# Kernel optimization log

Measured on AMD Instinct MI355X. Metric: run time of the kernel, lower is better.

## Reference

```python
import jax, jax.numpy as jnp
import numpy as np

B, S, D, H = 2, 2048, 1024, 16
DH = D // H

def setup_inputs() -> dict:
    key = jax.random.key(0)
    ks = jax.random.split(key, 12)
    inp = {
        'query': jax.random.normal(ks[0], (B, S, D), jnp.float32),
        'key':   jax.random.normal(ks[1], (B, S, D), jnp.float32),
        'value': jax.random.normal(ks[2], (B, S, D), jnp.float32),
        # causal mask: 1.0 where attention is DISALLOWED (added as mask * -1e9)
        'mask': jnp.triu(jnp.ones((S, S), jnp.float32), k=1)[None, None, :, :],
    }
    sc = 1.0 / np.sqrt(D)
    inp['Wq'] = jax.random.normal(ks[3], (D, D), jnp.float32) * sc
    inp['bq'] = jnp.zeros((D,), jnp.float32)
    inp['Wk'] = jax.random.normal(ks[4], (D, D), jnp.float32) * sc
    inp['bk'] = jnp.zeros((D,), jnp.float32)
    inp['Wv'] = jax.random.normal(ks[5], (D, D), jnp.float32) * sc
    inp['bv'] = jnp.zeros((D,), jnp.float32)
    inp['Wo'] = jax.random.normal(ks[6], (D, D), jnp.float32) * sc
    inp['bo'] = jnp.zeros((D,), jnp.float32)
    return inp

def _split_heads(x):
    # [B,S,D] -> [B,H,S,DH]
    b, s, _ = x.shape
    return x.reshape(b, s, H, DH).transpose(0, 2, 1, 3)

def reference(query, key, value, mask, Wq, bq, Wk, bk, Wv, bv, Wo, bo):
    q = _split_heads(query @ Wq + bq)
    k = _split_heads(key @ Wk + bk)
    v = _split_heads(value @ Wv + bv)
    scale = jnp.sqrt(jnp.asarray(DH, jnp.float32))
    # [B,H,S,S] score tensor (naive, unfused — matches original)
    score = jnp.einsum('bhqd,bhkd->bhqk', q, k) / scale
    score = score + mask * (-1e9)
    attn = jax.nn.softmax(score, axis=-1)
    ctx = jnp.einsum('bhqk,bhkd->bhqd', attn, v)
    ctx = ctx.transpose(0, 2, 1, 3).reshape(query.shape[0], -1, D)
    return ctx @ Wo + bo
```

## Files before the change

kernel.cpp:

```cpp
#include <hip/hip_runtime.h>
#include <hip/hip_bf16.h>
#include <stdint.h>


typedef __bf16 bf16;
typedef __bf16 bf16x2v __attribute__((ext_vector_type(2)));
typedef __bf16 bf16x4v __attribute__((ext_vector_type(4)));
typedef __bf16 bf16x8v __attribute__((ext_vector_type(8)));
typedef float  f32x4v  __attribute__((ext_vector_type(4)));
typedef float  f32x16v __attribute__((ext_vector_type(16)));
typedef unsigned int uint32x2v __attribute__((ext_vector_type(2)));

#define MFMA16(a, b, c) __builtin_amdgcn_mfma_f32_16x16x32_bf16((a), (b), (c), 0, 0, 0)
#define MFMA32(a, b, c) __builtin_amdgcn_mfma_f32_32x32x16_bf16((a), (b), (c), 0, 0, 0)

static constexpr int kS = 2048, kD = 1024, kH = 16, kDH = 64, kB = 2, kM = 4096;

__device__ __forceinline__ void gload16(const void* g, void* lds) {
  __builtin_amdgcn_global_load_lds((const __attribute__((address_space(1))) void*)g,
                                   (__attribute__((address_space(3))) void*)lds, 16, 0, 0);
}

__device__ __forceinline__ float fexp2(float x) {
#if __has_builtin(__builtin_amdgcn_exp2f)
  return __builtin_amdgcn_exp2f(x);
#else
  return exp2f(x);
#endif
}

__global__ void __launch_bounds__(256) cvt_x_kernel(
    const float* __restrict__ q, const float* __restrict__ k, const float* __restrict__ v,
    bf16* __restrict__ xq, bf16* __restrict__ xk, bf16* __restrict__ xv) {
  int i = (blockIdx.x * 256 + threadIdx.x) * 4;
  float4 a = *(const float4*)(q + i);
  float4 b = *(const float4*)(k + i);
  float4 c = *(const float4*)(v + i);
  bf16x4v oa = {(bf16)a.x, (bf16)a.y, (bf16)a.z, (bf16)a.w};
  bf16x4v ob = {(bf16)b.x, (bf16)b.y, (bf16)b.z, (bf16)b.w};
  bf16x4v oc = {(bf16)c.x, (bf16)c.y, (bf16)c.z, (bf16)c.w};
  *(bf16x4v*)(xq + i) = oa;
  *(bf16x4v*)(xk + i) = ob;
  *(bf16x4v*)(xv + i) = oc;
}

__global__ void __launch_bounds__(256) cvt_w_kernel(
    const float* __restrict__ w0, const float* __restrict__ w1,
    const float* __restrict__ w2, const float* __restrict__ w3,
    bf16* __restrict__ o0, bf16* __restrict__ o1, bf16* __restrict__ o2, bf16* __restrict__ o3) {
  const float* w = blockIdx.z == 0 ? w0 : blockIdx.z == 1 ? w1 : blockIdx.z == 2 ? w2 : w3;
  bf16* o       = blockIdx.z == 0 ? o0 : blockIdx.z == 1 ? o1 : blockIdx.z == 2 ? o2 : o3;
  __shared__ float t[32][33];
  int tx = threadIdx.x, ty = threadIdx.y;
  int k0 = blockIdx.x * 32, n0 = blockIdx.y * 32;
#pragma unroll
  for (int j = 0; j < 4; ++j)
    t[ty + j * 8][tx] = w[(size_t)(k0 + ty + j * 8) * kD + n0 + tx];
  __syncthreads();
#pragma unroll
  for (int j = 0; j < 4; ++j)
    o[(size_t)(n0 + ty + j * 8) * kD + k0 + tx] = (bf16)t[tx][ty + j * 8];
}

struct GemmArgs {
  const bf16* A;
  const bf16* Wt;
  const float* bias;
  void* out;
  float scale;
  int omode;
};

__global__ void __launch_bounds__(256) gemm_kernel(GemmArgs ga, GemmArgs gb, GemmArgs gc) {
  GemmArgs g = blockIdx.z == 0 ? ga : blockIdx.z == 1 ? gb : gc;
  __shared__ bf16 smem[8192];
  const int tid = threadIdx.x;
  const int wid = tid >> 6, lane = tid & 63;
  const int g4 = lane >> 4, l16 = lane & 15;
  const int m0 = blockIdx.x * 128, n0 = blockIdx.y * 128;
  const int wr = wid >> 1, wc = wid & 1;

  const int row0 = wid * 16 + (lane >> 2);
  const int row1 = 64 + row0;
  const int sw0 = (lane & 3) ^ ((row0 >> 1) & 3);
  const int sw1 = (lane & 3) ^ ((row1 >> 1) & 3);
  const bf16* gA0 = g.A + (size_t)(m0 + row0) * kD + sw0 * 8;
  const bf16* gA1 = g.A + (size_t)(m0 + row1) * kD + sw1 * 8;
  const bf16* gB0 = g.Wt + (size_t)(n0 + row0) * kD + sw0 * 8;
  const bf16* gB1 = g.Wt + (size_t)(n0 + row1) * kD + sw1 * 8;
  bf16* ldsA0 = &smem[wid * 512];
  bf16* ldsA1 = &smem[(4 + wid) * 512];
  bf16* ldsB0 = &smem[4096 + wid * 512];
  bf16* ldsB1 = &smem[4096 + (4 + wid) * 512];

  const int xorv = (l16 >> 1) & 3;
  f32x4v acc[4][4] = {};

  for (int k0 = 0; k0 < kD; k0 += 32) {
    __syncthreads();
    gload16(gA0 + k0, ldsA0);
    gload16(gA1 + k0, ldsA1);
    gload16(gB0 + k0, ldsB0);
    gload16(gB1 + k0, ldsB1);
    __syncthreads();
    bf16x8v af[4], bfr[4];
#pragma unroll
    for (int i = 0; i < 4; ++i) {
      int rowA = wr * 64 + i * 16 + l16;
      af[i] = *(const bf16x8v*)&smem[rowA * 32 + ((g4 ^ xorv) * 8)];
      int rowB = wc * 64 + i * 16 + l16;
      bfr[i] = *(const bf16x8v*)&smem[4096 + rowB * 32 + ((g4 ^ xorv) * 8)];
    }
#pragma unroll
    for (int i = 0; i < 4; ++i)
#pragma unroll
      for (int j = 0; j < 4; ++j)
        acc[i][j] = MFMA16(af[i], bfr[j], acc[i][j]);
  }

#pragma unroll
  for (int j = 0; j < 4; ++j) {
    int col = n0 + wc * 64 + j * 16 + l16;
    float bj = g.bias[col];
#pragma unroll
    for (int i = 0; i < 4; ++i) {
#pragma unroll
      for (int r = 0; r < 4; ++r) {
        int m = m0 + wr * 64 + i * 16 + g4 * 4 + r;
        float val = (acc[i][j][r] + bj) * g.scale;
        if (g.omode == 0) {
          ((float*)g.out)[(size_t)m * kD + col] = val;
        } else {
          int b = m >> 11, s = m & (kS - 1);
          int h = col >> 6, dh = col & 63;
          size_t addr = (g.omode == 1)
                            ? (((size_t)(b * kH + h) * kS + s) * kDH + dh)
                            : (((size_t)(b * kH + h) * kDH + dh) * kS + s);
          ((bf16*)g.out)[addr] = (bf16)val;
        }
      }
    }
  }
}

__global__ void __launch_bounds__(256) attn_kernel(
    const bf16* __restrict__ Qp, const bf16* __restrict__ Kp,
    const bf16* __restrict__ Vt, bf16* __restrict__ ctx) {
  __shared__ bf16 lds[16384];
  const int tid = threadIdx.x;
  const int wid = tid >> 6, lane = tid & 63;
  const int l32 = lane & 31, hi = lane >> 5;
  const int bh = blockIdx.x;
  const int qt = blockIdx.y;
  const int q0 = qt * 128;
  const int qw = q0 + wid * 32;
  const bf16* Qh = Qp + (size_t)bh * kS * kDH;
  const bf16* Kh = Kp + (size_t)bh * kS * kDH;
  const bf16* Vh = Vt + (size_t)bh * kDH * kS;

  bf16x8v qf[4];
#pragma unroll
  for (int kw = 0; kw < 4; ++kw)
    qf[kw] = *(const bf16x8v*)(Qh + (size_t)(qw + l32) * kDH + kw * 16 + hi * 8);

  f32x16v oacc[2] = {};
  float mreg = -1e30f, lsum = 0.f;
  const int q_lane = qw + l32;

  const int nt = (q0 >> 6) + 2;
  const int ntw = (qw >> 6) + 1;

  const int srow = lane >> 3, schk = lane & 7;
  auto stage = [&](int buf, int k0) {
    bf16* kd = &lds[buf * 8192];
    bf16* vd = kd + 4096;
#pragma unroll
    for (int i = 0; i < 2; ++i) {
      int r = wid * 16 + i * 8 + srow;
      int c = schk ^ (r & 7);
      gload16(Kh + (size_t)(k0 + r) * kDH + c * 8, kd + (wid * 2 + i) * 512);
      gload16(Vh + (size_t)r * kS + k0 + c * 8, vd + (wid * 2 + i) * 512);
    }
  };

  stage(0, 0);
  __syncthreads();
  int cur = 0;
  for (int t = 0; t < nt; ++t) {
    const int k0 = t * 64;
    if (t + 1 < nt) stage(cur ^ 1, k0 + 64);
    if (t < ntw) {
      const bf16* kb = &lds[cur * 8192];
      const bf16* vb = kb + 4096;
      f32x16v st[2] = {};
#pragma unroll
      for (int sub = 0; sub < 2; ++sub) {
        int row = sub * 32 + l32;
        const bf16* krow = kb + row * 64;
        int rx = row & 7;
#pragma unroll
        for (int kw = 0; kw < 4; ++kw) {
          int cw = kw * 2 + hi;
          bf16x8v af = *(const bf16x8v*)(krow + ((cw ^ rx) * 8));
          st[sub] = MFMA32(af, qf[kw], st[sub]);
        }
      }
      if (k0 + 63 > qw) {
#pragma unroll
        for (int sub = 0; sub < 2; ++sub)
#pragma unroll
          for (int r = 0; r < 16; ++r) {
            int kv = k0 + sub * 32 + (r & 3) + 8 * (r >> 2) + 4 * hi;
            if (kv > q_lane) st[sub][r] = -1e30f;
          }
      }
      float rm = st[0][0];
#pragma unroll
      for (int sub = 0; sub < 2; ++sub)
#pragma unroll
        for (int r = 0; r < 16; ++r) rm = fmaxf(rm, st[sub][r]);
      {
        uint32x2v sw = __builtin_amdgcn_permlane32_swap(
            __float_as_uint(rm), __float_as_uint(rm), false, false);
        float partner = __uint_as_float(hi ? sw.x : sw.y);
        rm = fmaxf(rm, partner);
      }
      float mn = fmaxf(mreg, rm);
      float al = fexp2(mreg - mn);
      mreg = mn;
      float rs = 0.f;
#pragma unroll
      for (int sub = 0; sub < 2; ++sub)
#pragma unroll
        for (int r = 0; r < 16; ++r) {
          st[sub][r] = fexp2(st[sub][r] - mn);
          rs += st[sub][r];
        }
      {
        uint32x2v sw = __builtin_amdgcn_permlane32_swap(
            __float_as_uint(rs), __float_as_uint(rs), false, false);
        rs += __uint_as_float(hi ? sw.x : sw.y);
      }
      lsum = lsum * al + rs;
#pragma unroll
      for (int s = 0; s < 2; ++s)
#pragma unroll
        for (int r = 0; r < 16; ++r) oacc[s][r] *= al;

      unsigned int w[16];
#pragma unroll
      for (int sub = 0; sub < 2; ++sub)
#pragma unroll
        for (int i = 0; i < 8; ++i) {
          union { bf16x2v h; unsigned int u; } cv;
          cv.h = bf16x2v{(bf16)st[sub][2 * i], (bf16)st[sub][2 * i + 1]};
          w[sub * 8 + i] = cv.u;
        }
      bf16x8v pb[4];
#pragma unroll
      for (int f = 0; f < 4; ++f) {
        uint32x2v r0 = __builtin_amdgcn_permlane32_swap(w[4 * f], w[4 * f + 2], false, false);
        uint32x2v r1 = __builtin_amdgcn_permlane32_swap(w[4 * f + 1], w[4 * f + 3], false, false);
        union { unsigned int u[4]; bf16x8v h; } fu;
        fu.u[0] = r0.x; fu.u[1] = r1.x; fu.u[2] = r0.y; fu.u[3] = r1.y;
        pb[f] = fu.h;
      }
#pragma unroll
      for (int f = 0; f < 4; ++f) {
        int cw = f * 2 + hi;
#pragma unroll
        for (int s = 0; s < 2; ++s) {
          int row = s * 32 + l32;
          bf16x8v vf = *(const bf16x8v*)(vb + row * 64 + ((cw ^ (row & 7)) * 8));
          oacc[s] = MFMA32(vf, pb[f], oacc[s]);
        }
      }
    }
    __syncthreads();
    cur ^= 1;
  }
  float inv = 1.0f / lsum;
  const int b = bh >> 4, h = bh & 15;
  bf16* crow = ctx + (size_t)(b * kS + qw + l32) * kD + h * 64;
#pragma unroll
  for (int s = 0; s < 2; ++s)
#pragma unroll
    for (int rq = 0; rq < 4; ++rq) {
      union { bf16x4v h; uint32x2v u; } pk;
      pk.h = bf16x4v{(bf16)(oacc[s][rq * 4 + 0] * inv), (bf16)(oacc[s][rq * 4 + 1] * inv),
                     (bf16)(oacc[s][rq * 4 + 2] * inv), (bf16)(oacc[s][rq * 4 + 3] * inv)};
      *(uint32x2v*)(crow + 8 * rq + 4 * hi + 32 * s) = pk.u;
    }
}

extern "C" void kernel_launch(void* const* d_in, const int* in_sizes, int n_in,
                              void* d_out, int out_size, void* d_ws, size_t ws_size,
                              hipStream_t stream) {
  (void)in_sizes; (void)n_in; (void)out_size; (void)ws_size;
  const float* q  = (const float*)d_in[0];
  const float* k  = (const float*)d_in[1];
  const float* v  = (const float*)d_in[2];
  const float* Wq = (const float*)d_in[4];
  const float* bq = (const float*)d_in[5];
  const float* Wk = (const float*)d_in[6];
  const float* bk = (const float*)d_in[7];
  const float* Wv = (const float*)d_in[8];
  const float* bv = (const float*)d_in[9];
  const float* Wo = (const float*)d_in[10];
  const float* bo = (const float*)d_in[11];

  char* p = (char*)d_ws;
  auto carve = [&](size_t bytes) {
    char* r = p;
    p += (bytes + 255) & ~(size_t)255;
    return r;
  };
  const size_t XB = (size_t)kM * kD * sizeof(bf16);
  const size_t WB = (size_t)kD * kD * sizeof(bf16);
  bf16* Xq  = (bf16*)carve(XB);
  bf16* Xk  = (bf16*)carve(XB);
  bf16* Xv  = (bf16*)carve(XB);
  bf16* Wtq = (bf16*)carve(WB);
  bf16* Wtk = (bf16*)carve(WB);
  bf16* Wtv = (bf16*)carve(WB);
  bf16* Wto = (bf16*)carve(WB);
  bf16* Qp  = (bf16*)carve(XB);
  bf16* Kp  = (bf16*)carve(XB);
  bf16* Vt  = (bf16*)carve(XB);
  bf16* Ctx = (bf16*)carve(XB);

  cvt_x_kernel<<<dim3(kM * kD / 1024), 256, 0, stream>>>(q, k, v, Xq, Xk, Xv);
  cvt_w_kernel<<<dim3(32, 32, 4), dim3(32, 8, 1), 0, stream>>>(Wq, Wk, Wv, Wo,
                                                               Wtq, Wtk, Wtv, Wto);
  GemmArgs aq{Xq, Wtq, bq, Qp, 0.125f * 1.44269504f, 1};
  GemmArgs ak{Xk, Wtk, bk, Kp, 1.0f, 1};
  GemmArgs av{Xv, Wtv, bv, Vt, 1.0f, 2};
  gemm_kernel<<<dim3(32, 8, 3), 256, 0, stream>>>(aq, ak, av);
  attn_kernel<<<dim3(32, 16), 256, 0, stream>>>(Qp, Kp, Vt, Ctx);
  GemmArgs ao{Ctx, Wto, bo, d_out, 1.0f, 0};
  gemm_kernel<<<dim3(32, 8, 1), 256, 0, stream>>>(ao, ao, ao);
}
```

Baseline: 243.2 us.

## Fuse fp32 activation cast into projection GEMM, stage epilogues, widen attention KV tiles

```diff
diff --git a/kernel.cpp b/kernel.cpp
--- a/kernel.cpp
+++ b/kernel.cpp
@@ -11,10 +11,11 @@
 typedef float  f32x16v __attribute__((ext_vector_type(16)));
 typedef unsigned int uint32x2v __attribute__((ext_vector_type(2)));
 
+#define MFMA32(a, b, c) __builtin_amdgcn_mfma_f32_32x32x16_bf16((a), (b), (c), 0, 0, 0)
 #define MFMA16(a, b, c) __builtin_amdgcn_mfma_f32_16x16x32_bf16((a), (b), (c), 0, 0, 0)
-#define MFMA32(a, b, c) __builtin_amdgcn_mfma_f32_32x32x16_bf16((a), (b), (c), 0, 0, 0)
-
-static constexpr int kS = 2048, kD = 1024, kH = 16, kDH = 64, kB = 2, kM = 4096;
+#define LGKM0() asm volatile("s_waitcnt lgkmcnt(0)" ::: "memory")
+
+static constexpr int kS = 2048, kD = 1024, kH = 16, kDH = 64, kM = 4096;
 
 __device__ __forceinline__ void gload16(const void* g, void* lds) {
   __builtin_amdgcn_global_load_lds((const __attribute__((address_space(1))) void*)g,
@@ -27,21 +28,6 @@
 #else
   return exp2f(x);
 #endif
-}
-
-__global__ void __launch_bounds__(256) cvt_x_kernel(
-    const float* __restrict__ q, const float* __restrict__ k, const float* __restrict__ v,
-    bf16* __restrict__ xq, bf16* __restrict__ xk, bf16* __restrict__ xv) {
-  int i = (blockIdx.x * 256 + threadIdx.x) * 4;
-  float4 a = *(const float4*)(q + i);
-  float4 b = *(const float4*)(k + i);
-  float4 c = *(const float4*)(v + i);
-  bf16x4v oa = {(bf16)a.x, (bf16)a.y, (bf16)a.z, (bf16)a.w};
-  bf16x4v ob = {(bf16)b.x, (bf16)b.y, (bf16)b.z, (bf16)b.w};
-  bf16x4v oc = {(bf16)c.x, (bf16)c.y, (bf16)c.z, (bf16)c.w};
-  *(bf16x4v*)(xq + i) = oa;
-  *(bf16x4v*)(xk + i) = ob;
-  *(bf16x4v*)(xv + i) = oc;
 }
 
 __global__ void __launch_bounds__(256) cvt_w_kernel(
@@ -63,7 +49,7 @@
 }
 
 struct GemmArgs {
-  const bf16* A;
+  const void* A;
   const bf16* Wt;
   const float* bias;
   void* out;
@@ -71,74 +57,160 @@
   int omode;
 };
 
+template <int BN, bool AFP32>
 __global__ void __launch_bounds__(256) gemm_kernel(GemmArgs ga, GemmArgs gb, GemmArgs gc) {
   GemmArgs g = blockIdx.z == 0 ? ga : blockIdx.z == 1 ? gb : gc;
-  __shared__ bf16 smem[8192];
-  const int tid = threadIdx.x;
-  const int wid = tid >> 6, lane = tid & 63;
+  constexpr int WN = BN / 2, NJ = WN / 16;
+  __shared__ __align__(16) char smem_raw[18432];
+  bf16* As = (bf16*)smem_raw;
+  bf16* Bs = (bf16*)(smem_raw + 8192);
+  const int tid = threadIdx.x, wid = tid >> 6, lane = tid & 63;
   const int g4 = lane >> 4, l16 = lane & 15;
-  const int m0 = blockIdx.x * 128, n0 = blockIdx.y * 128;
+  const int m0 = blockIdx.x * 128, n0 = blockIdx.y * BN;
   const int wr = wid >> 1, wc = wid & 1;
-
-  const int row0 = wid * 16 + (lane >> 2);
-  const int row1 = 64 + row0;
-  const int sw0 = (lane & 3) ^ ((row0 >> 1) & 3);
-  const int sw1 = (lane & 3) ^ ((row1 >> 1) & 3);
-  const bf16* gA0 = g.A + (size_t)(m0 + row0) * kD + sw0 * 8;
-  const bf16* gA1 = g.A + (size_t)(m0 + row1) * kD + sw1 * 8;
-  const bf16* gB0 = g.Wt + (size_t)(n0 + row0) * kD + sw0 * 8;
-  const bf16* gB1 = g.Wt + (size_t)(n0 + row1) * kD + sw1 * 8;
-  bf16* ldsA0 = &smem[wid * 512];
-  bf16* ldsA1 = &smem[(4 + wid) * 512];
-  bf16* ldsB0 = &smem[4096 + wid * 512];
-  bf16* ldsB1 = &smem[4096 + (4 + wid) * 512];
+  const bf16* Wt = g.Wt;
+
+  const int ar = tid >> 1, ah = tid & 1;
+  const float* gAf = (const float*)g.A + (size_t)(m0 + ar) * kD + ah * 16;
+  bf16* adst0 = As + ar * 32 + ((2 * ah) ^ ((ar >> 1) & 3)) * 8;
+  bf16* adst1 = As + ar * 32 + ((2 * ah + 1) ^ ((ar >> 1) & 3)) * 8;
 
   const int xorv = (l16 >> 1) & 3;
-  f32x4v acc[4][4] = {};
+  f32x4v acc[4][NJ] = {};
 
   for (int k0 = 0; k0 < kD; k0 += 32) {
     __syncthreads();
-    gload16(gA0 + k0, ldsA0);
-    gload16(gA1 + k0, ldsA1);
-    gload16(gB0 + k0, ldsB0);
-    gload16(gB1 + k0, ldsB1);
+    if constexpr (AFP32) {
+      float4 f0 = *(const float4*)(gAf + k0);
+      float4 f1 = *(const float4*)(gAf + k0 + 4);
+      float4 f2 = *(const float4*)(gAf + k0 + 8);
+      float4 f3 = *(const float4*)(gAf + k0 + 12);
+#pragma unroll
+      for (int i = 0; i < BN / 64; ++i) {
+        int id = i * 256 + tid;
+        int row = id >> 2, c = id & 3;
+        gload16(Wt + (size_t)(n0 + row) * kD + k0 + ((c ^ ((row >> 1) & 3)) * 8),
+                Bs + (i * 256 + wid * 64) * 8);
+      }
+      bf16x8v c0 = {(bf16)f0.x, (bf16)f0.y, (bf16)f0.z, (bf16)f0.w,
+                    (bf16)f1.x, (bf16)f1.y, (bf16)f1.z, (bf16)f1.w};
+      bf16x8v c1 = {(bf16)f2.x, (bf16)f2.y, (bf16)f2.z, (bf16)f2.w,
+                    (bf16)f3.x, (bf16)f3.y, (bf16)f3.z, (bf16)f3.w};
+      *(bf16x8v*)adst0 = c0;
+      *(bf16x8v*)adst1 = c1;
+    } else {
+      const bf16* Ab = (const bf16*)g.A;
+#pragma unroll
+      for (int i = 0; i < 2; ++i) {
+        int id = i * 256 + tid;
+        int row = id >> 2, c = id & 3;
+        gload16(Ab + (size_t)(m0 + row) * kD + k0 + ((c ^ ((row >> 1) & 3)) * 8),
+                As + (i * 256 + wid * 64) * 8);
+      }
+#pragma unroll
+      for (int i = 0; i < BN / 64; ++i) {
+        int id = i * 256 + tid;
+        int row = id >> 2, c = id & 3;
+        gload16(Wt + (size_t)(n0 + row) * kD + k0 + ((c ^ ((row >> 1) & 3)) * 8),
+                Bs + (i * 256 + wid * 64) * 8);
+      }
+    }
     __syncthreads();
-    bf16x8v af[4], bfr[4];
+    bf16x8v af[4], bfr[NJ];
 #pragma unroll
     for (int i = 0; i < 4; ++i) {
       int rowA = wr * 64 + i * 16 + l16;
-      af[i] = *(const bf16x8v*)&smem[rowA * 32 + ((g4 ^ xorv) * 8)];
-      int rowB = wc * 64 + i * 16 + l16;
-      bfr[i] = *(const bf16x8v*)&smem[4096 + rowB * 32 + ((g4 ^ xorv) * 8)];
+      af[i] = *(const bf16x8v*)(As + rowA * 32 + ((g4 ^ xorv) * 8));
+    }
+#pragma unroll
+    for (int j = 0; j < NJ; ++j) {
+      int rowB = wc * WN + j * 16 + l16;
+      bfr[j] = *(const bf16x8v*)(Bs + rowB * 32 + ((g4 ^ xorv) * 8));
     }
 #pragma unroll
     for (int i = 0; i < 4; ++i)
 #pragma unroll
-      for (int j = 0; j < 4; ++j)
+      for (int j = 0; j < NJ; ++j)
         acc[i][j] = MFMA16(af[i], bfr[j], acc[i][j]);
   }
 
-#pragma unroll
-  for (int j = 0; j < 4; ++j) {
-    int col = n0 + wc * 64 + j * 16 + l16;
-    float bj = g.bias[col];
+  __syncthreads();
+  float* bws = (float*)smem_raw + wid * 1152;
+  const int bb = m0 >> 11;
+
+  if (g.omode == 1) {
+    const int h = (n0 >> 6) + wc;
+    float bj[NJ];
+#pragma unroll
+    for (int j = 0; j < NJ; ++j) bj[j] = g.bias[n0 + wc * WN + j * 16 + l16];
 #pragma unroll
     for (int i = 0; i < 4; ++i) {
 #pragma unroll
-      for (int r = 0; r < 4; ++r) {
-        int m = m0 + wr * 64 + i * 16 + g4 * 4 + r;
-        float val = (acc[i][j][r] + bj) * g.scale;
-        if (g.omode == 0) {
-          ((float*)g.out)[(size_t)m * kD + col] = val;
-        } else {
-          int b = m >> 11, s = m & (kS - 1);
-          int h = col >> 6, dh = col & 63;
-          size_t addr = (g.omode == 1)
-                            ? (((size_t)(b * kH + h) * kS + s) * kDH + dh)
-                            : (((size_t)(b * kH + h) * kDH + dh) * kS + s);
-          ((bf16*)g.out)[addr] = (bf16)val;
-        }
-      }
+      for (int j = 0; j < NJ; ++j)
+#pragma unroll
+        for (int r = 0; r < 4; ++r)
+          bws[(g4 * 4 + r) * 68 + j * 16 + l16] = (acc[i][j][r] + bj[j]) * g.scale;
+      LGKM0();
+      int rr = lane & 15, q = lane >> 4;
+      const float* src = bws + rr * 68 + q * 16;
+      f32x4v v0 = *(const f32x4v*)(src);
+      f32x4v v1 = *(const f32x4v*)(src + 4);
+      f32x4v v2 = *(const f32x4v*)(src + 8);
+      f32x4v v3 = *(const f32x4v*)(src + 12);
+      bf16x8v o0 = {(bf16)v0.x, (bf16)v0.y, (bf16)v0.z, (bf16)v0.w,
+                    (bf16)v1.x, (bf16)v1.y, (bf16)v1.z, (bf16)v1.w};
+      bf16x8v o1 = {(bf16)v2.x, (bf16)v2.y, (bf16)v2.z, (bf16)v2.w,
+                    (bf16)v3.x, (bf16)v3.y, (bf16)v3.z, (bf16)v3.w};
+      int srow = m0 + wr * 64 + i * 16 + rr;
+      bf16* dst = (bf16*)g.out + ((size_t)(bb * kH + h) * kS + (srow & (kS - 1))) * kDH + q * 16;
+      *(bf16x8v*)dst = o0;
+      *(bf16x8v*)(dst + 8) = o1;
+      LGKM0();
+    }
+  } else if (g.omode == 2) {
+    const int h = (n0 >> 6) + wc;
+#pragma unroll
+    for (int j = 0; j < NJ; ++j) {
+      float bj = g.bias[n0 + wc * WN + j * 16 + l16];
+#pragma unroll
+      for (int i = 0; i < 4; ++i)
+#pragma unroll
+        for (int r = 0; r < 4; ++r)
+          bws[l16 * 72 + i * 16 + g4 * 4 + r] = acc[i][j][r] + bj;
+      LGKM0();
+#pragma unroll
+      for (int cc = 0; cc < 4; ++cc) {
+        int id = cc * 64 + lane;
+        int row = id >> 4, c = id & 15;
+        f32x4v v = *(const f32x4v*)(bws + row * 72 + c * 4);
+        bf16x4v ov = {(bf16)v.x, (bf16)v.y, (bf16)v.z, (bf16)v.w};
+        int dh = j * 16 + row;
+        int sg = m0 + wr * 64 + c * 4;
+        *(bf16x4v*)((bf16*)g.out +
+                    ((size_t)(bb * kH + h) * kDH + dh) * kS + (sg & (kS - 1))) = ov;
+      }
+      LGKM0();
+    }
+  } else {
+    float bj[NJ];
+#pragma unroll
+    for (int j = 0; j < NJ; ++j) bj[j] = g.bias[n0 + wc * WN + j * 16 + l16];
+#pragma unroll
+    for (int i = 0; i < 4; ++i) {
+#pragma unroll
+      for (int j = 0; j < NJ; ++j)
+#pragma unroll
+        for (int r = 0; r < 4; ++r)
+          bws[(g4 * 4 + r) * 36 + j * 16 + l16] = acc[i][j][r] + bj[j];
+      LGKM0();
+#pragma unroll
+      for (int cc = 0; cc < 2; ++cc) {
+        int row = lane >> 2, ch = cc * 4 + (lane & 3);
+        f32x4v v = *(const f32x4v*)(bws + row * 36 + ch * 4);
+        int srow = m0 + wr * 64 + i * 16 + row;
+        *(f32x4v*)((float*)g.out + (size_t)srow * kD + n0 + wc * WN + ch * 4) = v;
+      }
+      LGKM0();
     }
   }
 }
@@ -146,7 +218,7 @@
 __global__ void __launch_bounds__(256) attn_kernel(
     const bf16* __restrict__ Qp, const bf16* __restrict__ Kp,
     const bf16* __restrict__ Vt, bf16* __restrict__ ctx) {
-  __shared__ bf16 lds[16384];
+  __shared__ __align__(16) bf16 lds[32768];
   const int tid = threadIdx.x;
   const int wid = tid >> 6, lane = tid & 63;
   const int l32 = lane & 31, hi = lane >> 5;
@@ -167,19 +239,20 @@
   float mreg = -1e30f, lsum = 0.f;
   const int q_lane = qw + l32;
 
-  const int nt = (q0 >> 6) + 2;
-  const int ntw = (qw >> 6) + 1;
-
-  const int srow = lane >> 3, schk = lane & 7;
+  const int nt = qt + 1;
+
   auto stage = [&](int buf, int k0) {
-    bf16* kd = &lds[buf * 8192];
-    bf16* vd = kd + 4096;
-#pragma unroll
-    for (int i = 0; i < 2; ++i) {
-      int r = wid * 16 + i * 8 + srow;
-      int c = schk ^ (r & 7);
-      gload16(Kh + (size_t)(k0 + r) * kDH + c * 8, kd + (wid * 2 + i) * 512);
-      gload16(Vh + (size_t)r * kS + k0 + c * 8, vd + (wid * 2 + i) * 512);
+    bf16* kd = &lds[buf * 16384];
+    bf16* vd = kd + 8192;
+#pragma unroll
+    for (int i = 0; i < 4; ++i) {
+      int id = i * 256 + tid;
+      int kr = id >> 3, kc = id & 7;
+      gload16(Kh + (size_t)(k0 + kr) * kDH + ((kc ^ (kr & 7)) * 8),
+              kd + (i * 256 + wid * 64) * 8);
+      int vr = id >> 4, vc = id & 15;
+      gload16(Vh + (size_t)vr * kS + k0 + ((vc ^ (vr & 15)) * 8),
+              vd + (i * 256 + wid * 64) * 8);
     }
   };
 
@@ -187,98 +260,102 @@
   __syncthreads();
   int cur = 0;
   for (int t = 0; t < nt; ++t) {
-    const int k0 = t * 64;
-    if (t + 1 < nt) stage(cur ^ 1, k0 + 64);
-    if (t < ntw) {
-      const bf16* kb = &lds[cur * 8192];
-      const bf16* vb = kb + 4096;
-      f32x16v st[2] = {};
-#pragma unroll
-      for (int sub = 0; sub < 2; ++sub) {
+    const int k0 = t * 128;
+    if (t + 1 < nt) stage(cur ^ 1, k0 + 128);
+    const bf16* kb = &lds[cur * 16384];
+    const bf16* vb = kb + 8192;
+
+    bool live[4];
+#pragma unroll
+    for (int sub = 0; sub < 4; ++sub) live[sub] = (k0 + sub * 32 <= qw + 31);
+
+    f32x16v st[4];
+#pragma unroll
+    for (int sub = 0; sub < 4; ++sub) {
+      if (live[sub]) {
         int row = sub * 32 + l32;
         const bf16* krow = kb + row * 64;
         int rx = row & 7;
+        f32x16v s = {};
 #pragma unroll
         for (int kw = 0; kw < 4; ++kw) {
-          int cw = kw * 2 + hi;
-          bf16x8v af = *(const bf16x8v*)(krow + ((cw ^ rx) * 8));
-          st[sub] = MFMA32(af, qf[kw], st[sub]);
+          bf16x8v af = *(const bf16x8v*)(krow + (((kw * 2 + hi) ^ rx) * 8));
+          s = MFMA32(af, qf[kw], s);
         }
-      }
-      if (k0 + 63 > qw) {
-#pragma unroll
-        for (int sub = 0; sub < 2; ++sub)
+        st[sub] = s;
+      }
+    }
+    if (k0 + 127 > qw) {
+#pragma unroll
+      for (int sub = 0; sub < 4; ++sub)
+        if (live[sub])
 #pragma unroll
           for (int r = 0; r < 16; ++r) {
             int kv = k0 + sub * 32 + (r & 3) + 8 * (r >> 2) + 4 * hi;
             if (kv > q_lane) st[sub][r] = -1e30f;
           }
-      }
-      float rm = st[0][0];
-#pragma unroll
-      for (int sub = 0; sub < 2; ++sub)
+    }
+    float rm = -1e30f;
+#pragma unroll
+    for (int sub = 0; sub < 4; ++sub)
+      if (live[sub])
 #pragma unroll
         for (int r = 0; r < 16; ++r) rm = fmaxf(rm, st[sub][r]);
-      {
-        uint32x2v sw = __builtin_amdgcn_permlane32_swap(
-            __float_as_uint(rm), __float_as_uint(rm), false, false);
-        float partner = __uint_as_float(hi ? sw.x : sw.y);
-        rm = fmaxf(rm, partner);
-      }
-      float mn = fmaxf(mreg, rm);
-      float al = fexp2(mreg - mn);
-      mreg = mn;
-      float rs = 0.f;
-#pragma unroll
-      for (int sub = 0; sub < 2; ++sub)
-#pragma unroll
-        for (int r = 0; r < 16; ++r) {
-          st[sub][r] = fexp2(st[sub][r] - mn);
-          rs += st[sub][r];
-        }
-      {
-        uint32x2v sw = __builtin_amdgcn_permlane32_swap(
-            __float_as_uint(rs), __float_as_uint(rs), false, false);
-        rs += __uint_as_float(hi ? sw.x : sw.y);
-      }
-      lsum = lsum * al + rs;
-#pragma unroll
-      for (int s = 0; s < 2; ++s)
-#pragma unroll
-        for (int r = 0; r < 16; ++r) oacc[s][r] *= al;
-
-      unsigned int w[16];
-#pragma unroll
-      for (int sub = 0; sub < 2; ++sub)
+    {
+      uint32x2v sw = __builtin_amdgcn_permlane32_swap(
+          __float_as_uint(rm), __float_as_uint(rm), false, false);
+      rm = fmaxf(rm, __uint_as_float(hi ? sw.x : sw.y));
+    }
+    float mn = fmaxf(mreg, rm);
+    float al = fexp2(mreg - mn);
+    mreg = mn;
+    float rs = 0.f;
+    unsigned int w[32];
+#pragma unroll
+    for (int sub = 0; sub < 4; ++sub) {
+      if (live[sub]) {
 #pragma unroll
         for (int i = 0; i < 8; ++i) {
+          float p0 = fexp2(st[sub][2 * i] - mn);
+          float p1 = fexp2(st[sub][2 * i + 1] - mn);
+          rs += p0 + p1;
           union { bf16x2v h; unsigned int u; } cv;
-          cv.h = bf16x2v{(bf16)st[sub][2 * i], (bf16)st[sub][2 * i + 1]};
+          cv.h = bf16x2v{(bf16)p0, (bf16)p1};
           w[sub * 8 + i] = cv.u;
         }
-      bf16x8v pb[4];
-#pragma unroll
-      for (int f = 0; f < 4; ++f) {
+      }
+    }
+    {
+      uint32x2v sw = __builtin_amdgcn_permlane32_swap(
+          __float_as_uint(rs), __float_as_uint(rs), false, false);
+      rs += __uint_as_float(hi ? sw.x : sw.y);
+    }
+    lsum = lsum * al + rs;
+#pragma unroll
+    for (int s = 0; s < 2; ++s)
+#pragma unroll
+      for (int r = 0; r < 16; ++r) oacc[s][r] *= al;
+
+#pragma unroll
+    for (int f = 0; f < 8; ++f) {
+      if (k0 + f * 16 <= qw + 31) {
         uint32x2v r0 = __builtin_amdgcn_permlane32_swap(w[4 * f], w[4 * f + 2], false, false);
         uint32x2v r1 = __builtin_amdgcn_permlane32_swap(w[4 * f + 1], w[4 * f + 3], false, false);
         union { unsigned int u[4]; bf16x8v h; } fu;
         fu.u[0] = r0.x; fu.u[1] = r1.x; fu.u[2] = r0.y; fu.u[3] = r1.y;
-        pb[f] = fu.h;
-      }
-#pragma unroll
-      for (int f = 0; f < 4; ++f) {
         int cw = f * 2 + hi;
 #pragma unroll
         for (int s = 0; s < 2; ++s) {
           int row = s * 32 + l32;
-          bf16x8v vf = *(const bf16x8v*)(vb + row * 64 + ((cw ^ (row & 7)) * 8));
-          oacc[s] = MFMA32(vf, pb[f], oacc[s]);
+          bf16x8v vf = *(const bf16x8v*)(vb + row * 128 + ((cw ^ (row & 15)) * 8));
+          oacc[s] = MFMA32(vf, fu.h, oacc[s]);
         }
       }
     }
     __syncthreads();
     cur ^= 1;
   }
+
   float inv = 1.0f / lsum;
   const int b = bh >> 4, h = bh & 15;
   bf16* crow = ctx + (size_t)(b * kS + qw + l32) * kD + h * 64;
@@ -317,9 +394,6 @@
   };
   const size_t XB = (size_t)kM * kD * sizeof(bf16);
   const size_t WB = (size_t)kD * kD * sizeof(bf16);
-  bf16* Xq  = (bf16*)carve(XB);
-  bf16* Xk  = (bf16*)carve(XB);
-  bf16* Xv  = (bf16*)carve(XB);
   bf16* Wtq = (bf16*)carve(WB);
   bf16* Wtk = (bf16*)carve(WB);
   bf16* Wtv = (bf16*)carve(WB);
@@ -329,14 +403,13 @@
   bf16* Vt  = (bf16*)carve(XB);
   bf16* Ctx = (bf16*)carve(XB);
 
-  cvt_x_kernel<<<dim3(kM * kD / 1024), 256, 0, stream>>>(q, k, v, Xq, Xk, Xv);
   cvt_w_kernel<<<dim3(32, 32, 4), dim3(32, 8, 1), 0, stream>>>(Wq, Wk, Wv, Wo,
                                                                Wtq, Wtk, Wtv, Wto);
-  GemmArgs aq{Xq, Wtq, bq, Qp, 0.125f * 1.44269504f, 1};
-  GemmArgs ak{Xk, Wtk, bk, Kp, 1.0f, 1};
-  GemmArgs av{Xv, Wtv, bv, Vt, 1.0f, 2};
-  gemm_kernel<<<dim3(32, 8, 3), 256, 0, stream>>>(aq, ak, av);
+  GemmArgs aq{q, Wtq, bq, Qp, 0.125f * 1.44269504f, 1};
+  GemmArgs ak{k, Wtk, bk, Kp, 1.0f, 1};
+  GemmArgs av{v, Wtv, bv, Vt, 1.0f, 2};
+  gemm_kernel<128, true><<<dim3(32, 8, 3), 256, 0, stream>>>(aq, ak, av);
   attn_kernel<<<dim3(32, 16), 256, 0, stream>>>(Qp, Kp, Vt, Ctx);
   GemmArgs ao{Ctx, Wto, bo, d_out, 1.0f, 0};
-  gemm_kernel<<<dim3(32, 8, 1), 256, 0, stream>>>(ao, ao, ao);
-}
+  gemm_kernel<64, false><<<dim3(32, 16, 1), 256, 0, stream>>>(ao, ao, ao);
+}
```

Measured after the change: 309.7 us. 1.27x slower.
